# Performance work log

Hardware: AMD Instinct MI355X
Metric: run time of the kernel (lower is better)

The kernel has to match this reference:

```python
import jax, jax.numpy as jnp
import numpy as np

FILTER_SIZE = 8
INPUT_DIM = 128
KERNEL_SIZE = 256


def setup_inputs() -> dict:
    key = jax.random.key(0)
    k1, k2, k3, k4 = jax.random.split(key, 4)
    user_batch = jax.random.normal(k1, (32, 2048, INPUT_DIM), dtype=jnp.float32)
    # Params initialized like torch.rand (uniform [0,1))
    filt = jax.random.uniform(k2, (FILTER_SIZE, INPUT_DIM), dtype=jnp.float32)
    W_k = jax.random.uniform(k3, (FILTER_SIZE * INPUT_DIM, KERNEL_SIZE), dtype=jnp.float32)
    b_k = jax.random.uniform(k4, (KERNEL_SIZE,), dtype=jnp.float32)
    return {"user_batch": user_batch, "filt": filt, "W_k": W_k, "b_k": b_k}


def reference(user_batch, filt, W_k, b_k):
    B, L, D = user_batch.shape
    F = filt.shape[0]
    n_win = L - F  # NOTE: original loop is range(0, L - F): exactly L - F windows
    # Gather sliding windows: [B, n_win, F, D]
    idx = jnp.arange(n_win)[:, None] + jnp.arange(F)[None, :]
    windows = user_batch[:, idx, :]
    # Elementwise mul with filter then contract flattened (F*D) against W_k
    W = W_k.reshape(F, D, -1)  # [F, D, K]
    out = jnp.einsum('blfd,fd,fdk->blk', windows, filt, W)
    return jax.nn.relu(out + b_k)
```

## Files before the change

### kernel.cpp

```cpp
#include <hip/hip_runtime.h>


#define L_SZ   2048
#define NWIN   2040
#define BM     128
#define MT     16

typedef __attribute__((ext_vector_type(8)))  short bf16x8;
typedef __attribute__((ext_vector_type(4)))  short bf16x4;
typedef __attribute__((ext_vector_type(16))) float f32x16;

static __device__ __forceinline__ short f2bf(float f) {
    union { float f; unsigned u; } v; v.f = f;
    unsigned r = v.u + 0x7FFFu + ((v.u >> 16) & 1u);
    return (short)(r >> 16);
}

__global__ __launch_bounds__(256) void prep_w_kernel(
    const float* __restrict__ Wk, const float* __restrict__ filt,
    short* __restrict__ wp3)
{
    int g   = blockIdx.x * 256 + threadIdx.x;
    int c   = g >> 10;
    int nb  = (g >> 7) & 7;
    int c8  = (g >> 5) & 3;
    int l32 = g & 31;
    int np  = nb * 32 + l32;
    int kb  = c * 32 + c8 * 8;
    bf16x8 o;
    #pragma unroll
    for (int jj = 0; jj < 8; ++jj)
        o[jj] = f2bf(Wk[(size_t)(kb + jj) * 256 + np] * filt[kb + jj]);
    *reinterpret_cast<bf16x8*>(&wp3[(size_t)g * 8]) = o;
}

__global__ __launch_bounds__(512, 4) void cnn_enc_kernel(
    const float* __restrict__ ub, const short* __restrict__ wp3,
    const float* __restrict__ bk, float* __restrict__ out)
{
    __shared__ short sA[135 * 136];

    const int tid   = threadIdx.x;
    const int bid   = blockIdx.x;
    const int mt    = bid & 15;
    const int batch = bid >> 4;
    const int l0    = mt * BM;

    const int lane = tid & 63;
    const int wave = tid >> 6;
    const int wm   = wave >> 2;
    const int wn   = wave & 3;
    const int l32  = lane & 31;
    const int half = lane >> 5;

    const float* ubb = ub + ((size_t)batch << 18);
    float4 av[9];
    #pragma unroll
    for (int u = 0; u < 9; ++u) {
        int idx = tid + u * 512;
        if (u < 8 || idx < 4320) {
            int r  = idx >> 5;
            int c4 = idx & 31;
            int rg = l0 + r; if (rg > L_SZ - 1) rg = L_SZ - 1;
            av[u] = *reinterpret_cast<const float4*>(
                ubb + ((size_t)rg << 7) + c4 * 4);
        }
    }
    #pragma unroll
    for (int u = 0; u < 9; ++u) {
        int idx = tid + u * 512;
        if (u < 8 || idx < 4320) {
            int r  = idx >> 5;
            int c4 = idx & 31;
            bf16x4 o;
            o.x = f2bf(av[u].x); o.y = f2bf(av[u].y);
            o.z = f2bf(av[u].z); o.w = f2bf(av[u].w);
            *reinterpret_cast<bf16x4*>(&sA[r * 136 + c4 * 4]) = o;
        }
    }

    f32x16 acc[2][2];
    #pragma unroll
    for (int i = 0; i < 2; ++i)
        #pragma unroll
        for (int j = 0; j < 2; ++j)
            acc[i][j] = (f32x16){0.f,0.f,0.f,0.f,0.f,0.f,0.f,0.f,
                                 0.f,0.f,0.f,0.f,0.f,0.f,0.f,0.f};

    int aoff[2];
    #pragma unroll
    for (int i = 0; i < 2; ++i)
        aoff[i] = (wm * 64 + i * 32 + l32) * 136 + half * 8;

    const short* wb = wp3 + (size_t)(wn * 2) * 1024 + (size_t)lane * 8;
    auto loadB = [&](bf16x8 (&b)[2][2], int c) {
        #pragma unroll
        for (int ks = 0; ks < 2; ++ks)
            #pragma unroll
            for (int j = 0; j < 2; ++j)
                b[ks][j] = *reinterpret_cast<const bf16x8*>(
                    wb + (size_t)c * 8192 + j * 1024 + ks * 512);
    };

    auto kstep = [&](int c, bf16x8 (&b)[2][2]) {
        const int f = c >> 2, ds = c & 3;
        bf16x8 a[2][2];
        #pragma unroll
        for (int ks = 0; ks < 2; ++ks)
            #pragma unroll
            for (int i = 0; i < 2; ++i)
                a[ks][i] = *reinterpret_cast<const bf16x8*>(
                    &sA[aoff[i] + f * 136 + ds * 32 + ks * 16]);
        __builtin_amdgcn_s_setprio(1);
        #pragma unroll
        for (int ks = 0; ks < 2; ++ks)
            #pragma unroll
            for (int i = 0; i < 2; ++i)
                #pragma unroll
                for (int j = 0; j < 2; ++j)
                    acc[i][j] = __builtin_amdgcn_mfma_f32_32x32x16_bf16(
                        a[ks][i], b[ks][j], acc[i][j], 0, 0, 0);
        __builtin_amdgcn_s_setprio(0);
    };

    bf16x8 bA[2][2], bB[2][2];
    loadB(bA, 0);
    __syncthreads();

    #pragma unroll 1
    for (int c = 0; c < 32; c += 2) {
        loadB(bB, c + 1);
        kstep(c, bA);
        if (c < 30) loadB(bA, c + 2);
        kstep(c + 1, bB);
    }

    #pragma unroll
    for (int j = 0; j < 2; ++j) {
        int n_glob = wn * 64 + j * 32 + l32;
        float bias = bk[n_glob];
        #pragma unroll
        for (int i = 0; i < 2; ++i) {
            #pragma unroll
            for (int r = 0; r < 16; ++r) {
                int row = (r & 3) + 8 * (r >> 2) + 4 * half;
                int l = l0 + wm * 64 + i * 32 + row;
                if (l < NWIN) {
                    float v = acc[i][j][r] + bias;
                    __builtin_nontemporal_store(
                        v > 0.f ? v : 0.f,
                        &out[((size_t)batch * NWIN + l) * 256 + n_glob]);
                }
            }
        }
    }
}

extern "C" void kernel_launch(void* const* d_in, const int* in_sizes, int n_in,
                              void* d_out, int out_size, void* d_ws, size_t ws_size,
                              hipStream_t stream) {
    const float* ub   = (const float*)d_in[0];
    const float* filt = (const float*)d_in[1];
    const float* Wk   = (const float*)d_in[2];
    const float* bk   = (const float*)d_in[3];
    float* out = (float*)d_out;
    short* wp3 = (short*)d_ws;

    hipLaunchKernelGGL(prep_w_kernel, dim3(128), dim3(256), 0, stream,
                       Wk, filt, wp3);
    hipLaunchKernelGGL(cnn_enc_kernel, dim3(32 * MT), dim3(512), 0, stream,
                       ub, wp3, bk, out);
}
```

Baseline: 129.0 us.

## Stage weight tiles into LDS via async global_load_lds with 4-deep ring buffer

Replaces per-wave register loads of the pre-packed weight matrix with direct global-to-LDS async loads into a 4-slot ring buffer, shared by all waves in the block. The prep kernel's layout is changed to match. The main loop now handles one 16-wide k-step per iteration with a barrier per step. The aim is to cut redundant global loads of B (each wave previously fetched its own copy) and to overlap fetches with MFMA. The cost is a block-wide barrier every iteration, extra LDS use that may lower occupancy, and smaller MFMA batches per sync.

```diff
diff --git a/kernel.cpp b/kernel.cpp
--- a/kernel.cpp
+++ b/kernel.cpp
@@ -16,29 +16,35 @@
     return (short)(r >> 16);
 }
 
+static __device__ __forceinline__ void gload_lds16(const short* g, short* l) {
+    __builtin_amdgcn_global_load_lds(
+        (const __attribute__((address_space(1))) unsigned int*)g,
+        (__attribute__((address_space(3))) unsigned int*)l, 16, 0, 0);
+}
+
 __global__ __launch_bounds__(256) void prep_w_kernel(
     const float* __restrict__ Wk, const float* __restrict__ filt,
-    short* __restrict__ wp3)
+    short* __restrict__ wp4)
 {
-    int g   = blockIdx.x * 256 + threadIdx.x;
-    int c   = g >> 10;
-    int nb  = (g >> 7) & 7;
-    int c8  = (g >> 5) & 3;
-    int l32 = g & 31;
-    int np  = nb * 32 + l32;
-    int kb  = c * 32 + c8 * 8;
+    int g    = blockIdx.x * 256 + threadIdx.x;
+    int c16  = g >> 9;
+    int s    = g & 511;
+    int half = s >> 8;
+    int n    = s & 255;
+    int kb   = c16 * 16 + half * 8;
     bf16x8 o;
     #pragma unroll
     for (int jj = 0; jj < 8; ++jj)
-        o[jj] = f2bf(Wk[(size_t)(kb + jj) * 256 + np] * filt[kb + jj]);
-    *reinterpret_cast<bf16x8*>(&wp3[(size_t)g * 8]) = o;
+        o[jj] = f2bf(Wk[(size_t)(kb + jj) * 256 + n] * filt[kb + jj]);
+    *reinterpret_cast<bf16x8*>(&wp4[(size_t)g * 8]) = o;
 }
 
 __global__ __launch_bounds__(512, 4) void cnn_enc_kernel(
-    const float* __restrict__ ub, const short* __restrict__ wp3,
+    const float* __restrict__ ub, const short* __restrict__ wp4,
     const float* __restrict__ bk, float* __restrict__ out)
 {
     __shared__ short sA[135 * 136];
+    __shared__ short sB[4 * 4096];
 
     const int tid   = threadIdx.x;
     const int bid   = blockIdx.x;
@@ -53,6 +59,11 @@
     const int l32  = lane & 31;
     const int half = lane >> 5;
 
+    auto stageB = [&](int c) {
+        const short* src = wp4 + (size_t)c * 4096 + (size_t)(wave * 64 + lane) * 8;
+        gload_lds16(src, &sB[(c & 3) * 4096 + wave * 512]);
+    };
+
     const float* ubb = ub + ((size_t)batch << 18);
     float4 av[9];
     #pragma unroll
@@ -66,6 +77,7 @@
                 ubb + ((size_t)rg << 7) + c4 * 4);
         }
     }
+    stageB(0); stageB(1); stageB(2);
     #pragma unroll
     for (int u = 0; u < 9; ++u) {
         int idx = tid + u * 512;
@@ -91,48 +103,35 @@
     #pragma unroll
     for (int i = 0; i < 2; ++i)
         aoff[i] = (wm * 64 + i * 32 + l32) * 136 + half * 8;
+    const int boff = (half * 256 + wn * 64 + l32) * 8;
 
-    const short* wb = wp3 + (size_t)(wn * 2) * 1024 + (size_t)lane * 8;
-    auto loadB = [&](bf16x8 (&b)[2][2], int c) {
-        #pragma unroll
-        for (int ks = 0; ks < 2; ++ks)
-            #pragma unroll
-            for (int j = 0; j < 2; ++j)
-                b[ks][j] = *reinterpret_cast<const bf16x8*>(
-                    wb + (size_t)c * 8192 + j * 1024 + ks * 512);
-    };
-
-    auto kstep = [&](int c, bf16x8 (&b)[2][2]) {
-        const int f = c >> 2, ds = c & 3;
-        bf16x8 a[2][2];
-        #pragma unroll
-        for (int ks = 0; ks < 2; ++ks)
-            #pragma unroll
-            for (int i = 0; i < 2; ++i)
-                a[ks][i] = *reinterpret_cast<const bf16x8*>(
-                    &sA[aoff[i] + f * 136 + ds * 32 + ks * 16]);
-        __builtin_amdgcn_s_setprio(1);
-        #pragma unroll
-        for (int ks = 0; ks < 2; ++ks)
-            #pragma unroll
-            for (int i = 0; i < 2; ++i)
-                #pragma unroll
-                for (int j = 0; j < 2; ++j)
-                    acc[i][j] = __builtin_amdgcn_mfma_f32_32x32x16_bf16(
-                        a[ks][i], b[ks][j], acc[i][j], 0, 0, 0);
-        __builtin_amdgcn_s_setprio(0);
-    };
-
-    bf16x8 bA[2][2], bB[2][2];
-    loadB(bA, 0);
-    __syncthreads();
+    asm volatile("s_waitcnt vmcnt(2) lgkmcnt(0)" ::: "memory");
+    __builtin_amdgcn_s_barrier();
+    __builtin_amdgcn_sched_barrier(0);
 
     #pragma unroll 1
-    for (int c = 0; c < 32; c += 2) {
-        loadB(bB, c + 1);
-        kstep(c, bA);
-        if (c < 30) loadB(bA, c + 2);
-        kstep(c + 1, bB);
+    for (int c = 0; c < 64; ++c) {
+        const int f = c >> 3, dsub = c & 7;
+        const int bb = (c & 3) * 4096;
+        bf16x8 a0 = *reinterpret_cast<const bf16x8*>(
+            &sA[aoff[0] + f * 136 + dsub * 16]);
+        bf16x8 a1 = *reinterpret_cast<const bf16x8*>(
+            &sA[aoff[1] + f * 136 + dsub * 16]);
+        bf16x8 b0 = *reinterpret_cast<const bf16x8*>(&sB[bb + boff]);
+        bf16x8 b1 = *reinterpret_cast<const bf16x8*>(&sB[bb + boff + 256]);
+        if (c < 63) {
+            if (c < 62) asm volatile("s_waitcnt vmcnt(1)" ::: "memory");
+            else        asm volatile("s_waitcnt vmcnt(0)" ::: "memory");
+            __builtin_amdgcn_s_barrier();
+            __builtin_amdgcn_sched_barrier(0);
+            if (c < 61) stageB(c + 3);
+        }
+        __builtin_amdgcn_s_setprio(1);
+        acc[0][0] = __builtin_amdgcn_mfma_f32_32x32x16_bf16(a0, b0, acc[0][0], 0, 0, 0);
+        acc[0][1] = __builtin_amdgcn_mfma_f32_32x32x16_bf16(a0, b1, acc[0][1], 0, 0, 0);
+        acc[1][0] = __builtin_amdgcn_mfma_f32_32x32x16_bf16(a1, b0, acc[1][0], 0, 0, 0);
+        acc[1][1] = __builtin_amdgcn_mfma_f32_32x32x16_bf16(a1, b1, acc[1][1], 0, 0, 0);
+        __builtin_amdgcn_s_setprio(0);
     }
 
     #pragma unroll
@@ -164,10 +163,10 @@
     const float* Wk   = (const float*)d_in[2];
     const float* bk   = (const float*)d_in[3];
     float* out = (float*)d_out;
-    short* wp3 = (short*)d_ws;
+    short* wp4 = (short*)d_ws;
 
     hipLaunchKernelGGL(prep_w_kernel, dim3(128), dim3(256), 0, stream,
-                       Wk, filt, wp3);
+                       Wk, filt, wp4);
     hipLaunchKernelGGL(cnn_enc_kernel, dim3(32 * MT), dim3(512), 0, stream,
-                       ub, wp3, bk, out);
+                       ub, wp4, bk, out);
 }
```

After: 124.7 us. 1.03x faster.
